# Kernel optimization log

Measured on AMD Instinct MI355X. Metric: run time of the kernel, lower is better.

The kernel has to match this reference:

```python
import jax, jax.numpy as jnp
import numpy as np

N, E = 768, 24576
NODE_DIM, EDGE_DIM, HID = 8, 4, 8
MLP_HID = 4 * HID  # 32


def _mlp(x, params):
    # torch nn.Linear: y = x @ W.T + b; ReLU after every layer except the last
    *hidden, last = params
    for W, b in hidden:
        x = jax.nn.relu(x @ W.T + b)
    W, b = last
    return x @ W.T + b


def _init_mlp(key, dims):
    params = []
    for din, dout in zip(dims[:-1], dims[1:]):
        key, k1, k2 = jax.random.split(key, 3)
        lim = 1.0 / np.sqrt(din)
        W = jax.random.uniform(k1, (dout, din), minval=-lim, maxval=lim, dtype=jnp.float32)
        b = jax.random.uniform(k2, (dout,), minval=-lim, maxval=lim, dtype=jnp.float32)
        params.append((W, b))
    return params


def setup_inputs() -> dict:
    key = jax.random.key(0)
    k_mtr, k_feat, k_ei, k_ea, k_emlp, k_omlp = jax.random.split(key, 6)
    inp = {
        "mtr": jax.random.normal(k_mtr, (N, N, HID), dtype=jnp.float32),
        "feat": jax.random.normal(k_feat, (N, NODE_DIM), dtype=jnp.float32),
        "edge_index": jax.random.randint(k_ei, (2, E), 0, N, dtype=jnp.int64),
        "edge_attr": jax.random.normal(k_ea, (E, EDGE_DIM), dtype=jnp.float32),
    }
    edge_in_dim = EDGE_DIM + 2 * NODE_DIM              # 20
    out_in_dim = 2 * HID + 2 * NODE_DIM + 1            # 33
    eparams = _init_mlp(k_emlp, [edge_in_dim, MLP_HID, MLP_HID, MLP_HID, HID * HID])
    oparams = _init_mlp(k_omlp, [out_in_dim, MLP_HID, MLP_HID, MLP_HID, HID])
    for i, (W, b) in enumerate(eparams):
        inp[f"e_w{i}"], inp[f"e_b{i}"] = W, b
    for i, (W, b) in enumerate(oparams):
        inp[f"o_w{i}"], inp[f"o_b{i}"] = W, b
    return inp


def reference(mtr, feat, edge_index, edge_attr,
              e_w0, e_b0, e_w1, e_b1, e_w2, e_b2, e_w3, e_b3,
              o_w0, o_b0, o_w1, o_b1, o_w2, o_b2, o_w3, o_b3):
    n, h = mtr.shape[0], mtr.shape[2]
    eparams = [(e_w0, e_b0), (e_w1, e_b1), (e_w2, e_b2), (e_w3, e_b3)]
    oparams = [(o_w0, o_b0), (o_w1, o_b1), (o_w2, o_b2), (o_w3, o_b3)]
    src, dst = edge_index[0], edge_index[1]
    # edge MLP on [E, edge_dim + 2*node_dim]
    edge_in = jnp.concatenate([edge_attr, feat[src], feat[dst]], axis=-1)
    evals = _mlp(edge_in, eparams).reshape(-1, h, h)  # [E, h, h]
    # scatter into dense [n, n, h, h] adjacency tensor (zeros for non-edges)
    fmtr = jnp.zeros((n, n, h, h), dtype=mtr.dtype).at[src, dst].set(evals)
    # walk contraction over (j, c)
    mtr1 = jnp.einsum('ijc,jkct->ikt', mtr, fmtr) / h  # [n, n, h]
    eye = jnp.eye(n, dtype=mtr.dtype)[:, :, None]                       # [n, n, 1]
    feat_j = jnp.broadcast_to(feat[None, :, :], (n, n, feat.shape[-1]))  # row-broadcast
    feat_i = jnp.broadcast_to(feat[:, None, :], (n, n, feat.shape[-1]))  # col-broadcast
    cat = jnp.concatenate(
        [mtr1, jnp.transpose(mtr1, (1, 0, 2)), feat_j, feat_i, eye], axis=-1)  # [n, n, 33]
    return mtr + _mlp(cat, oparams)
```

## Files before the change

### kernel.cpp

```cpp
#include <hip/hip_runtime.h>

#define N 768
#define E 24576
#define NPAD_SLOTS (E + 3 * 768)
#define NGROUPS (NPAD_SLOTS / 4)

typedef __attribute__((ext_vector_type(8))) short bf16x8;
typedef __attribute__((ext_vector_type(4))) float f32x4;

__device__ __forceinline__ unsigned pk2(float lo, float hi) {
  unsigned r;
  asm("v_cvt_pk_bf16_f32 %0, %1, %2" : "=v"(r) : "v"(lo), "v"(hi));
  return r;
}

union FragU {
  unsigned u[4];
  bf16x8 s;
};

__device__ __forceinline__ bf16x8 pack_frag(float4 a, float4 b) {
  FragU f;
  f.u[0] = pk2(a.x, a.y);
  f.u[1] = pk2(a.z, a.w);
  f.u[2] = pk2(b.x, b.y);
  f.u[3] = pk2(b.z, b.w);
  return f.s;
}

__device__ __forceinline__ bf16x8 relu_pack(f32x4 d1, f32x4 d2) {
  FragU f;
  f.u[0] = pk2(fmaxf(d1[0], 0.f), fmaxf(d1[1], 0.f));
  f.u[1] = pk2(fmaxf(d1[2], 0.f), fmaxf(d1[3], 0.f));
  f.u[2] = pk2(fmaxf(d2[0], 0.f), fmaxf(d2[1], 0.f));
  f.u[3] = pk2(fmaxf(d2[2], 0.f), fmaxf(d2[3], 0.f));
  return f.s;
}

__device__ __forceinline__ f32x4 ld4(const float* p) {
  float4 v = *(const float4*)p;
  f32x4 r;
  r[0] = v.x; r[1] = v.y; r[2] = v.z; r[3] = v.w;
  return r;
}

__global__ __launch_bounds__(256) void prep0(
    const float* __restrict__ mtr, uint4* __restrict__ mtrT,
    int4* __restrict__ winner4, uint4* __restrict__ Mfrag4,
    int* __restrict__ jlist, int* __restrict__ deg, int* __restrict__ curs,
    int* __restrict__ done_ctr) {
  __shared__ float lds[16][16 * 8 + 4];
  if (blockIdx.x < 2304) {
    const int r = threadIdx.x >> 4;
    const int c = threadIdx.x & 15;
    const size_t j0 = (size_t)(blockIdx.x % 48) * 16;
    const size_t i0 = (size_t)(blockIdx.x / 48) * 16;

    const float4* src = (const float4*)(mtr + ((i0 + r) * N + (j0 + c)) * 8);
    float4 a = src[0], b = src[1];
    *(float4*)&lds[r][c * 8 + 0] = a;
    *(float4*)&lds[r][c * 8 + 4] = b;
    __syncthreads();
    float4 ta = *(float4*)&lds[c][r * 8 + 0];
    float4 tb = *(float4*)&lds[c][r * 8 + 4];
    uint4 o;
    o.x = pk2(ta.x, ta.y); o.y = pk2(ta.z, ta.w);
    o.z = pk2(tb.x, tb.y); o.w = pk2(tb.z, tb.w);
    mtrT[(j0 + r) * N + (i0 + c)] = o;
  } else {
    const int t = (blockIdx.x - 2304) * 256 + threadIdx.x;
    Mfrag4[t] = make_uint4(0, 0, 0, 0);
    if (t < 147456) winner4[t] = make_int4(-1, -1, -1, -1);
    if (t < NPAD_SLOTS) jlist[t] = 0;
    if (t < 1024) { deg[t] = 0; curs[t] = 0; }
    if (t == 0) *done_ctr = 0;
  }
}

__global__ __launch_bounds__(256) void edge_prep_scan(
    const int* __restrict__ ei, int* __restrict__ winner,
    int* __restrict__ deg, int* __restrict__ offs,
    int* __restrict__ done_ctr) {
  const int e = blockIdx.x * 256 + threadIdx.x;
  const int s = ei[e];
  const int d = ei[E + e];
  atomicMax(&winner[(size_t)s * N + d], e);
  atomicAdd(&deg[d], 1);

  __threadfence();
  __syncthreads();
  __shared__ int ticket;
  if (threadIdx.x == 0) ticket = atomicAdd(done_ctr, 1);
  __syncthreads();
  if (ticket == (E / 256) - 1 && threadIdx.x < 64) {
    const int lane = threadIdx.x;
    int v[12];
    int sum = 0;
#pragma unroll
    for (int z = 0; z < 12; ++z) {
      v[z] = (atomicAdd(&deg[lane * 12 + z], 0) + 3) & ~3;
      sum += v[z];
    }
    int inc = sum;
#pragma unroll
    for (int dd = 1; dd < 64; dd <<= 1) {
      int t = __shfl_up(inc, dd, 64);
      if (lane >= dd) inc += t;
    }
    int run = inc - sum;
#pragma unroll
    for (int z = 0; z < 12; ++z) {
      run += v[z];
      offs[lane * 12 + z + 1] = run;
    }
    if (lane == 0) offs[0] = 0;
  }
}

__global__ __launch_bounds__(256) void edge_mlp_mfma(
    const float* __restrict__ feat, const int* __restrict__ ei,
    const float* __restrict__ ea, const int* __restrict__ winner,
    const int* __restrict__ offs, int* __restrict__ curs,
    int* __restrict__ jlist,
    const float* __restrict__ w0, const float* __restrict__ b0,
    const float* __restrict__ w1, const float* __restrict__ b1,
    const float* __restrict__ w2, const float* __restrict__ b2,
    const float* __restrict__ w3, const float* __restrict__ b3,
    short* __restrict__ Mfrag) {
  __shared__ float Ld[4][16 * 65];
  const int wv = threadIdx.x >> 6;
  const int lane = threadIdx.x & 63;
  const int col = lane & 15;
  const int hi = lane >> 4;
  const int e = (blockIdx.x * 4 + wv) * 16 + col;

  const float4 z4 = make_float4(0.f, 0.f, 0.f, 0.f);

  const int s = ei[e];
  const int d = ei[E + e];
  int pos = -1;
  if (hi == 0) {
    if (winner[(size_t)s * N + d] == e) {
      pos = offs[d] + atomicAdd(&curs[d], 1);
      jlist[pos] = s;
    }
  }
  pos = __shfl(pos, col, 64);

  const float* pa = (hi == 0) ? (ea + (size_t)e * 4)
                  : (hi == 1) ? (feat + (size_t)s * 8)
                  : (hi == 2) ? (feat + (size_t)s * 8 + 4)
                              : (feat + (size_t)d * 8);
  float4 va = *(const float4*)pa;
  float4 vb = (hi == 0) ? *(const float4*)(feat + (size_t)d * 8 + 4) : z4;
  bf16x8 bfr = pack_frag(va, vb);

  bf16x8 a0lo, a0hi, a1lo, a1hi, a2lo, a2hi, a3f[4];
  {
    const float* p = w0 + col * 20;
    float4 xa = *(const float4*)(p + hi * 4);
    float4 xb = (hi == 0) ? *(const float4*)(p + 16) : z4;
    a0lo = pack_frag(xa, xb);
    const float* q = w0 + (col + 16) * 20;
    float4 ya = *(const float4*)(q + hi * 4);
    float4 yb = (hi == 0) ? *(const float4*)(q + 16) : z4;
    a0hi = pack_frag(ya, yb);
  }
  a1lo = pack_frag(*(const float4*)(w1 + col * 32 + hi * 4),
                   *(const float4*)(w1 + col * 32 + 16 + hi * 4));
  a1hi = pack_frag(*(const float4*)(w1 + (col + 16) * 32 + hi * 4),
                   *(const float4*)(w1 + (col + 16) * 32 + 16 + hi * 4));
  a2lo = pack_frag(*(const float4*)(w2 + col * 32 + hi * 4),
                   *(const float4*)(w2 + col * 32 + 16 + hi * 4));
  a2hi = pack_frag(*(const float4*)(w2 + (col + 16) * 32 + hi * 4),
                   *(const float4*)(w2 + (col + 16) * 32 + 16 + hi * 4));
#pragma unroll
  for (int q = 0; q < 4; ++q) {
    const float* p = w3 + (size_t)(q * 16 + col) * 32;
    a3f[q] = pack_frag(*(const float4*)(p + hi * 4),
                       *(const float4*)(p + 16 + hi * 4));
  }

  f32x4 d1 = ld4(b0 + hi * 4), d2 = ld4(b0 + 16 + hi * 4);
  d1 = __builtin_amdgcn_mfma_f32_16x16x32_bf16(a0lo, bfr, d1, 0, 0, 0);
  d2 = __builtin_amdgcn_mfma_f32_16x16x32_bf16(a0hi, bfr, d2, 0, 0, 0);
  bfr = relu_pack(d1, d2);

  d1 = ld4(b1 + hi * 4); d2 = ld4(b1 + 16 + hi * 4);
  d1 = __builtin_amdgcn_mfma_f32_16x16x32_bf16(a1lo, bfr, d1, 0, 0, 0);
  d2 = __builtin_amdgcn_mfma_f32_16x16x32_bf16(a1hi, bfr, d2, 0, 0, 0);
  bfr = relu_pack(d1, d2);

  d1 = ld4(b2 + hi * 4); d2 = ld4(b2 + 16 + hi * 4);
  d1 = __builtin_amdgcn_mfma_f32_16x16x32_bf16(a2lo, bfr, d1, 0, 0, 0);
  d2 = __builtin_amdgcn_mfma_f32_16x16x32_bf16(a2hi, bfr, d2, 0, 0, 0);
  bfr = relu_pack(d1, d2);

#pragma unroll
  for (int q = 0; q < 4; ++q) {
    f32x4 d3 = ld4(b3 + q * 16 + hi * 4);
    d3 = __builtin_amdgcn_mfma_f32_16x16x32_bf16(a3f[q], bfr, d3, 0, 0, 0);
#pragma unroll
    for (int r = 0; r < 4; ++r)
      Ld[wv][col * 65 + q * 16 + hi * 4 + r] = d3[r];
  }
  __syncthreads();

  if (pos >= 0) {
    const int gid = pos >> 2;
    const int sg = pos & 3;
    short* base = Mfrag + (size_t)gid * 512 + (sg & 1) * 256 + (sg >> 1) * 4;
    const int hl = hi >> 1;
    const int t0 = (hi & 1) * 4;
    const float* m = &Ld[wv][col * 65];
#pragma unroll
    for (int cc = 0; cc < 4; ++cc) {
      const int t = t0 + cc;
      unsigned u0 = pk2(m[(hl * 4 + 0) * 8 + t], m[(hl * 4 + 1) * 8 + t]);
      unsigned u1 = pk2(m[(hl * 4 + 2) * 8 + t], m[(hl * 4 + 3) * 8 + t]);
      *(uint2*)(base + hl * 128 + t * 8) = make_uint2(u0, u1);
    }
  }
}

__global__ __launch_bounds__(256) void contract7(
    const short* __restrict__ mtrT, const short* __restrict__ Mfrag,
    const int* __restrict__ jlist, const int* __restrict__ offs,
    const int* __restrict__ wcnt, short* __restrict__ WTb) {
  __shared__ float sD[4][4][16][9];

  const int bid = blockIdx.x;
  const int g = (bid & 7) * 288 + (bid >> 3);
  const int ig = g / 768;
  const int k = g % 768;
  const int w = threadIdx.x >> 6;
  const int lane = threadIdx.x & 63;
  const int col = lane & 15;
  const int hi = lane >> 4;
  const int ibase = ig * 256 + w * 64;

  const int base = offs[k];
  const int cnt = wcnt[k];
  const int ngr = (cnt + 3) >> 2;

  f32x4 acc0 = {0.f, 0.f, 0.f, 0.f}, acc1 = {0.f, 0.f, 0.f, 0.f};
  f32x4 acc2 = {0.f, 0.f, 0.f, 0.f}, acc3 = {0.f, 0.f, 0.f, 0.f};

  const size_t lane_off = ((size_t)(ibase + col)) * 8 + (hi & 1) * 4;

#pragma unroll 1
  for (int gg = 0; gg < ngr; ++gg) {
    const int4 js = *(const int4*)(jlist + base + gg * 4);
    const int ja = (hi & 2) ? js.y : js.x;
    const int jb = (hi & 2) ? js.w : js.z;

    bf16x8 bfr = *(const bf16x8*)(
        Mfrag + ((size_t)(base >> 2) + gg) * 512 + lane * 8);

    const short* pa = mtrT + (size_t)ja * (N * 8) + lane_off;
    const short* pb = mtrT + (size_t)jb * (N * 8) + lane_off;

#define TILE(ACC, T)                                                     \
  do {                                                                   \
    uint2 ua = *(const uint2*)(pa + (T) * (16 * 8));                     \
    uint2 ub = *(const uint2*)(pb + (T) * (16 * 8));                     \
    FragU af;                                                            \
    af.u[0] = ua.x; af.u[1] = ua.y; af.u[2] = ub.x; af.u[3] = ub.y;      \
    ACC = __builtin_amdgcn_mfma_f32_16x16x32_bf16(af.s, bfr, ACC, 0, 0, 0); \
  } while (0)

    TILE(acc0, 0);
    TILE(acc1, 1);
    TILE(acc2, 2);
    TILE(acc3, 3);
#undef TILE
  }

  if (col < 8) {
#pragma unroll
    for (int r = 0; r < 4; ++r) {
      sD[w][0][hi * 4 + r][col] = acc0[r] * 0.125f;
      sD[w][1][hi * 4 + r][col] = acc1[r] * 0.125f;
      sD[w][2][hi * 4 + r][col] = acc2[r] * 0.125f;
      sD[w][3][hi * 4 + r][col] = acc3[r] * 0.125f;
    }
  }
  __syncthreads();
  if (lane < 16) {
#pragma unroll
    for (int t = 0; t < 4; ++t) {
      const float* row = &sD[w][t][lane][0];
      uint4 o;
      o.x = pk2(row[0], row[1]); o.y = pk2(row[2], row[3]);
      o.z = pk2(row[4], row[5]); o.w = pk2(row[6], row[7]);
      *(uint4*)(WTb + ((size_t)k * N + ibase + t * 16 + lane) * 8) = o;
    }
  }
}

__global__ __launch_bounds__(256, 2) void out_mlp_mfma(
    const float* __restrict__ mtr, const short* __restrict__ WTb,
    const float* __restrict__ feat,
    const float* __restrict__ w0, const float* __restrict__ b0,
    const float* __restrict__ w1, const float* __restrict__ b1,
    const float* __restrict__ w2, const float* __restrict__ b2,
    const float* __restrict__ w3, const float* __restrict__ b3,
    float* __restrict__ out) {
  const int i = blockIdx.x;
  const int w = threadIdx.x >> 6;
  const int col = threadIdx.x & 15;
  const int hi = (threadIdx.x >> 4) & 3;

  bf16x8 a0lo, a0hi, a1lo, a1hi, a2lo, a2hi, a3;
  {
    const float* p = w0 + col * 33;
    float4 xa = make_float4(p[hi * 4], p[hi * 4 + 1], p[hi * 4 + 2], p[hi * 4 + 3]);
    float4 xb = make_float4(p[16 + hi * 4], p[16 + hi * 4 + 1],
                            p[16 + hi * 4 + 2], p[16 + hi * 4 + 3]);
    a0lo = pack_frag(xa, xb);
    const float* q = w0 + (col + 16) * 33;
    float4 ya = make_float4(q[hi * 4], q[hi * 4 + 1], q[hi * 4 + 2], q[hi * 4 + 3]);
    float4 yb = make_float4(q[16 + hi * 4], q[16 + hi * 4 + 1],
                            q[16 + hi * 4 + 2], q[16 + hi * 4 + 3]);
    a0hi = pack_frag(ya, yb);
  }
  a1lo = pack_frag(*(const float4*)(w1 + col * 32 + hi * 4),
                   *(const float4*)(w1 + col * 32 + 16 + hi * 4));
  a1hi = pack_frag(*(const float4*)(w1 + (col + 16) * 32 + hi * 4),
                   *(const float4*)(w1 + (col + 16) * 32 + 16 + hi * 4));
  a2lo = pack_frag(*(const float4*)(w2 + col * 32 + hi * 4),
                   *(const float4*)(w2 + col * 32 + 16 + hi * 4));
  a2hi = pack_frag(*(const float4*)(w2 + (col + 16) * 32 + hi * 4),
                   *(const float4*)(w2 + (col + 16) * 32 + 16 + hi * 4));
  if (col < 8) {
    a3 = pack_frag(*(const float4*)(w3 + col * 32 + hi * 4),
                   *(const float4*)(w3 + col * 32 + 16 + hi * 4));
  } else {
    FragU z; z.u[0] = z.u[1] = z.u[2] = z.u[3] = 0; a3 = z.s;
  }

  const f32x4 c1a = ld4(b0 + hi * 4), c1b = ld4(b0 + 16 + hi * 4);
  const f32x4 c2a = ld4(b1 + hi * 4), c2b = ld4(b1 + 16 + hi * 4);
  const f32x4 c3a = ld4(b2 + hi * 4), c3b = ld4(b2 + 16 + hi * 4);
  f32x4 c4;
  if (hi < 2) c4 = ld4(b3 + hi * 4);
  else { c4[0] = c4[1] = c4[2] = c4[3] = 0.f; }

  float dg1[4], dg2[4];
#pragma unroll
  for (int r = 0; r < 4; ++r) {
    dg1[r] = w0[(hi * 4 + r) * 33 + 32];
    dg2[r] = w0[(16 + hi * 4 + r) * 33 + 32];
  }

#pragma unroll 1
  for (int g = 0; g < 12; ++g) {
    const int krow = w * 192 + g * 16 + col;

    FragU bf;
    const short* pW = (hi < 2)
        ? (WTb + ((size_t)krow * N + i) * 8 + (hi & 1) * 4)
        : (WTb + ((size_t)i * N + krow) * 8 + (hi & 1) * 4);
    uint2 wv2 = *(const uint2*)pW;
    const float* pF = (hi < 2) ? (feat + (size_t)krow * 8 + (hi & 1) * 4)
                               : (feat + (size_t)i * 8 + (hi & 1) * 4);
    float4 fv = *(const float4*)pF;
    bf.u[0] = wv2.x; bf.u[1] = wv2.y;
    bf.u[2] = pk2(fv.x, fv.y); bf.u[3] = pk2(fv.z, fv.w);
    bf16x8 bfr = bf.s;

    f32x4 d1 = c1a, d2 = c1b;
    d1 = __builtin_amdgcn_mfma_f32_16x16x32_bf16(a0lo, bfr, d1, 0, 0, 0);
    d2 = __builtin_amdgcn_mfma_f32_16x16x32_bf16(a0hi, bfr, d2, 0, 0, 0);
    const float eye = (krow == i) ? 1.f : 0.f;
#pragma unroll
    for (int r = 0; r < 4; ++r) {
      d1[r] = fmaf(eye, dg1[r], d1[r]);
      d2[r] = fmaf(eye, dg2[r], d2[r]);
    }
    bfr = relu_pack(d1, d2);

    d1 = c2a; d2 = c2b;
    d1 = __builtin_amdgcn_mfma_f32_16x16x32_bf16(a1lo, bfr, d1, 0, 0, 0);
    d2 = __builtin_amdgcn_mfma_f32_16x16x32_bf16(a1hi, bfr, d2, 0, 0, 0);
    bfr = relu_pack(d1, d2);

    d1 = c3a; d2 = c3b;
    d1 = __builtin_amdgcn_mfma_f32_16x16x32_bf16(a2lo, bfr, d1, 0, 0, 0);
    d2 = __builtin_amdgcn_mfma_f32_16x16x32_bf16(a2hi, bfr, d2, 0, 0, 0);
    bfr = relu_pack(d1, d2);

    f32x4 d3 = c4;
    d3 = __builtin_amdgcn_mfma_f32_16x16x32_bf16(a3, bfr, d3, 0, 0, 0);

    if (hi < 2) {
      const size_t idx = ((size_t)i * N + krow) * 8 + hi * 4;
      float4 m = *(const float4*)(mtr + idx);
      *(float4*)(out + idx) =
          make_float4(m.x + d3[0], m.y + d3[1], m.z + d3[2], m.w + d3[3]);
    }
  }
}

extern "C" void kernel_launch(void* const* d_in, const int* in_sizes, int n_in,
                              void* d_out, int out_size, void* d_ws,
                              size_t ws_size, hipStream_t stream) {
  const float* mtr  = (const float*)d_in[0];
  const float* feat = (const float*)d_in[1];
  const int*   ei   = (const int*)d_in[2];
  const float* ea   = (const float*)d_in[3];
  const float* ew0 = (const float*)d_in[4];
  const float* eb0 = (const float*)d_in[5];
  const float* ew1 = (const float*)d_in[6];
  const float* eb1 = (const float*)d_in[7];
  const float* ew2 = (const float*)d_in[8];
  const float* eb2 = (const float*)d_in[9];
  const float* ew3 = (const float*)d_in[10];
  const float* eb3 = (const float*)d_in[11];
  const float* ow0 = (const float*)d_in[12];
  const float* ob0 = (const float*)d_in[13];
  const float* ow1 = (const float*)d_in[14];
  const float* ob1 = (const float*)d_in[15];
  const float* ow2 = (const float*)d_in[16];
  const float* ob2 = (const float*)d_in[17];
  const float* ow3 = (const float*)d_in[18];
  const float* ob3 = (const float*)d_in[19];
  float* out = (float*)d_out;

  char* ws = (char*)d_ws;
  short* Mfrag = (short*)ws; ws += (size_t)NGROUPS * 512 * 2;
  short* mtrT  = (short*)ws; ws += (size_t)N * N * 8 * 2;
  short* WTb   = (short*)ws; ws += (size_t)N * N * 8 * 2;
  int* winner  = (int*)ws;   ws += (size_t)N * N * 4;
  int* deg     = (int*)ws;   ws += 1024 * 4;
  int* offs    = (int*)ws;   ws += 1024 * 4;
  int* curs    = (int*)ws;   ws += 1024 * 4;
  int* done_ctr = (int*)ws;  ws += 256 * 4;
  int* jlist   = (int*)ws;   ws += (size_t)NPAD_SLOTS * 4;

  prep0<<<2304 + 1680, 256, 0, stream>>>(mtr, (uint4*)mtrT, (int4*)winner,
                                         (uint4*)Mfrag, jlist, deg, curs,
                                         done_ctr);
  edge_prep_scan<<<E / 256, 256, 0, stream>>>(ei, winner, deg, offs, done_ctr);
  edge_mlp_mfma<<<E / 64, 256, 0, stream>>>(feat, ei, ea, winner, offs, curs,
                                            jlist, ew0, eb0, ew1, eb1, ew2,
                                            eb2, ew3, eb3, Mfrag);
  contract7<<<2304, 256, 0, stream>>>(mtrT, Mfrag, jlist, offs, curs, WTb);
  out_mlp_mfma<<<N, 256, 0, stream>>>(mtr, WTb, feat, ow0, ob0, ow1, ob1, ow2,
                                      ob2, ow3, ob3, out);
}
```

Measured before the change: 91.08 us.

## Fuse contraction and output MLP into persistent kernel with grid barrier and prefetch

Merges the contract and out_mlp kernels into one persistent kernel of 768 blocks. Each block does three contraction work items, then waits at a software grid barrier built from atomics before running the output MLP. The contraction loop now software-pipelines its gathers of the j-list, mtrT and Mfrag one group ahead. The MLP loop prefetches the WTb, feat and residual mtr values for the next row group. This removes one launch and hides load latency, but the spin barrier assumes all 768 blocks are resident at once (launch bounds of 3 per CU), and a larger register footprint may reduce occupancy.

```diff
diff --git a/kernel.cpp b/kernel.cpp
--- a/kernel.cpp
+++ b/kernel.cpp
@@ -4,6 +4,7 @@
 #define E 24576
 #define NPAD_SLOTS (E + 3 * 768)
 #define NGROUPS (NPAD_SLOTS / 4)
+#define TAIL_NB 768
 
 typedef __attribute__((ext_vector_type(8))) short bf16x8;
 typedef __attribute__((ext_vector_type(4))) float f32x4;
@@ -44,11 +45,25 @@
   return r;
 }
 
+__device__ __forceinline__ void grid_barrier(int* cnt, int* flag) {
+  __syncthreads();
+  __threadfence();
+  if (threadIdx.x == 0) {
+    if (atomicAdd(cnt, 1) == TAIL_NB - 1) {
+      atomicExch(flag, 1);
+    } else {
+      while (atomicAdd(flag, 0) == 0) __builtin_amdgcn_s_sleep(16);
+    }
+  }
+  __syncthreads();
+  __threadfence();
+}
+
 __global__ __launch_bounds__(256) void prep0(
     const float* __restrict__ mtr, uint4* __restrict__ mtrT,
     int4* __restrict__ winner4, uint4* __restrict__ Mfrag4,
     int* __restrict__ jlist, int* __restrict__ deg, int* __restrict__ curs,
-    int* __restrict__ done_ctr) {
+    int* __restrict__ ctrs) {
   __shared__ float lds[16][16 * 8 + 4];
   if (blockIdx.x < 2304) {
     const int r = threadIdx.x >> 4;
@@ -73,7 +88,7 @@
     if (t < 147456) winner4[t] = make_int4(-1, -1, -1, -1);
     if (t < NPAD_SLOTS) jlist[t] = 0;
     if (t < 1024) { deg[t] = 0; curs[t] = 0; }
-    if (t == 0) *done_ctr = 0;
+    if (t < 8) ctrs[t] = 0;
   }
 }
 
@@ -223,93 +238,120 @@
   }
 }
 
-__global__ __launch_bounds__(256) void contract7(
+__global__ __launch_bounds__(256, 3) void tail_fused(
     const short* __restrict__ mtrT, const short* __restrict__ Mfrag,
     const int* __restrict__ jlist, const int* __restrict__ offs,
-    const int* __restrict__ wcnt, short* __restrict__ WTb) {
+    const int* __restrict__ wcnt, short* __restrict__ WTb,
+    const float* __restrict__ mtr, const float* __restrict__ feat,
+    const float* __restrict__ w0, const float* __restrict__ b0,
+    const float* __restrict__ w1, const float* __restrict__ b1,
+    const float* __restrict__ w2, const float* __restrict__ b2,
+    const float* __restrict__ w3, const float* __restrict__ b3,
+    float* __restrict__ out, int* __restrict__ bar_cnt,
+    int* __restrict__ bar_flag) {
   __shared__ float sD[4][4][16][9];
 
-  const int bid = blockIdx.x;
-  const int g = (bid & 7) * 288 + (bid >> 3);
-  const int ig = g / 768;
-  const int k = g % 768;
   const int w = threadIdx.x >> 6;
   const int lane = threadIdx.x & 63;
   const int col = lane & 15;
   const int hi = lane >> 4;
-  const int ibase = ig * 256 + w * 64;
-
-  const int base = offs[k];
-  const int cnt = wcnt[k];
-  const int ngr = (cnt + 3) >> 2;
-
-  f32x4 acc0 = {0.f, 0.f, 0.f, 0.f}, acc1 = {0.f, 0.f, 0.f, 0.f};
-  f32x4 acc2 = {0.f, 0.f, 0.f, 0.f}, acc3 = {0.f, 0.f, 0.f, 0.f};
-
-  const size_t lane_off = ((size_t)(ibase + col)) * 8 + (hi & 1) * 4;
 
 #pragma unroll 1
-  for (int gg = 0; gg < ngr; ++gg) {
-    const int4 js = *(const int4*)(jlist + base + gg * 4);
-    const int ja = (hi & 2) ? js.y : js.x;
-    const int jb = (hi & 2) ? js.w : js.z;
-
-    bf16x8 bfr = *(const bf16x8*)(
-        Mfrag + ((size_t)(base >> 2) + gg) * 512 + lane * 8);
-
-    const short* pa = mtrT + (size_t)ja * (N * 8) + lane_off;
-    const short* pb = mtrT + (size_t)jb * (N * 8) + lane_off;
-
-#define TILE(ACC, T)                                                     \
-  do {                                                                   \
-    uint2 ua = *(const uint2*)(pa + (T) * (16 * 8));                     \
-    uint2 ub = *(const uint2*)(pb + (T) * (16 * 8));                     \
-    FragU af;                                                            \
-    af.u[0] = ua.x; af.u[1] = ua.y; af.u[2] = ub.x; af.u[3] = ub.y;      \
-    ACC = __builtin_amdgcn_mfma_f32_16x16x32_bf16(af.s, bfr, ACC, 0, 0, 0); \
+  for (int it = 0; it < 3; ++it) {
+    const int vb = blockIdx.x + it * TAIL_NB;
+    const int g = (vb & 7) * 288 + (vb >> 3);
+    const int ig = g / 768;
+    const int k = g % 768;
+    const int ibase = ig * 256 + w * 64;
+
+    const int base = offs[k];
+    const int cnt = wcnt[k];
+    const int ngr = (cnt + 3) >> 2;
+
+    f32x4 acc0 = {0.f, 0.f, 0.f, 0.f}, acc1 = {0.f, 0.f, 0.f, 0.f};
+    f32x4 acc2 = {0.f, 0.f, 0.f, 0.f}, acc3 = {0.f, 0.f, 0.f, 0.f};
+
+    const size_t lane_off = ((size_t)(ibase + col)) * 8 + (hi & 1) * 4;
+    const short* Mf = Mfrag + (size_t)(base >> 2) * 512 + lane * 8;
+
+#define LOADA(JS, AA, AB)                                               \
+  do {                                                                  \
+    const int _ja = (hi & 2) ? (JS).y : (JS).x;                         \
+    const int _jb = (hi & 2) ? (JS).w : (JS).z;                         \
+    const short* _pa = mtrT + (size_t)_ja * (N * 8) + lane_off;         \
+    const short* _pb = mtrT + (size_t)_jb * (N * 8) + lane_off;         \
+    _Pragma("unroll") for (int t = 0; t < 4; ++t) {                     \
+      AA[t] = *(const uint2*)(_pa + t * 128);                           \
+      AB[t] = *(const uint2*)(_pb + t * 128);                           \
+    }                                                                   \
   } while (0)
 
-    TILE(acc0, 0);
-    TILE(acc1, 1);
-    TILE(acc2, 2);
-    TILE(acc3, 3);
+    uint2 Aa0[4], Ab0[4], Aa1[4], Ab1[4];
+    bf16x8 mb0, mb1;
+    int4 js1 = make_int4(0, 0, 0, 0);
+
+    {
+      int4 js0 = *(const int4*)(jlist + base);
+      if (ngr > 1) js1 = *(const int4*)(jlist + base + 4);
+      LOADA(js0, Aa0, Ab0);
+      mb0 = *(const bf16x8*)(Mf);
+    }
+
+#pragma unroll 1
+    for (int gg = 0; gg < ngr; ++gg) {
+      int4 js2 = js1;
+      if (gg + 2 < ngr) js2 = *(const int4*)(jlist + base + (gg + 2) * 4);
+      if (gg + 1 < ngr) {
+        LOADA(js1, Aa1, Ab1);
+        mb1 = *(const bf16x8*)(Mf + (size_t)(gg + 1) * 512);
+      }
+
+#define TILE(ACC, T)                                                       \
+  do {                                                                    \
+    FragU af;                                                             \
+    af.u[0] = Aa0[T].x; af.u[1] = Aa0[T].y;                               \
+    af.u[2] = Ab0[T].x; af.u[3] = Ab0[T].y;                               \
+    ACC = __builtin_amdgcn_mfma_f32_16x16x32_bf16(af.s, mb0, ACC, 0, 0, 0); \
+  } while (0)
+      TILE(acc0, 0);
+      TILE(acc1, 1);
+      TILE(acc2, 2);
+      TILE(acc3, 3);
 #undef TILE
-  }
-
-  if (col < 8) {
-#pragma unroll
-    for (int r = 0; r < 4; ++r) {
-      sD[w][0][hi * 4 + r][col] = acc0[r] * 0.125f;
-      sD[w][1][hi * 4 + r][col] = acc1[r] * 0.125f;
-      sD[w][2][hi * 4 + r][col] = acc2[r] * 0.125f;
-      sD[w][3][hi * 4 + r][col] = acc3[r] * 0.125f;
-    }
-  }
-  __syncthreads();
-  if (lane < 16) {
-#pragma unroll
-    for (int t = 0; t < 4; ++t) {
-      const float* row = &sD[w][t][lane][0];
-      uint4 o;
-      o.x = pk2(row[0], row[1]); o.y = pk2(row[2], row[3]);
-      o.z = pk2(row[4], row[5]); o.w = pk2(row[6], row[7]);
-      *(uint4*)(WTb + ((size_t)k * N + ibase + t * 16 + lane) * 8) = o;
-    }
-  }
-}
-
-__global__ __launch_bounds__(256, 2) void out_mlp_mfma(
-    const float* __restrict__ mtr, const short* __restrict__ WTb,
-    const float* __restrict__ feat,
-    const float* __restrict__ w0, const float* __restrict__ b0,
-    const float* __restrict__ w1, const float* __restrict__ b1,
-    const float* __restrict__ w2, const float* __restrict__ b2,
-    const float* __restrict__ w3, const float* __restrict__ b3,
-    float* __restrict__ out) {
+
+      js1 = js2;
+#pragma unroll
+      for (int t = 0; t < 4; ++t) { Aa0[t] = Aa1[t]; Ab0[t] = Ab1[t]; }
+      mb0 = mb1;
+    }
+#undef LOADA
+
+    if (col < 8) {
+#pragma unroll
+      for (int r = 0; r < 4; ++r) {
+        sD[w][0][hi * 4 + r][col] = acc0[r] * 0.125f;
+        sD[w][1][hi * 4 + r][col] = acc1[r] * 0.125f;
+        sD[w][2][hi * 4 + r][col] = acc2[r] * 0.125f;
+        sD[w][3][hi * 4 + r][col] = acc3[r] * 0.125f;
+      }
+    }
+    __syncthreads();
+    if (lane < 16) {
+#pragma unroll
+      for (int t = 0; t < 4; ++t) {
+        const float* row = &sD[w][t][lane][0];
+        uint4 o;
+        o.x = pk2(row[0], row[1]); o.y = pk2(row[2], row[3]);
+        o.z = pk2(row[4], row[5]); o.w = pk2(row[6], row[7]);
+        *(uint4*)(WTb + ((size_t)k * N + ibase + t * 16 + lane) * 8) = o;
+      }
+    }
+    __syncthreads();
+  }
+
+  grid_barrier(bar_cnt, bar_flag);
+
   const int i = blockIdx.x;
-  const int w = threadIdx.x >> 6;
-  const int col = threadIdx.x & 15;
-  const int hi = (threadIdx.x >> 4) & 3;
 
   bf16x8 a0lo, a0hi, a1lo, a1hi, a2lo, a2hi, a3;
   {
@@ -353,18 +395,36 @@
     dg2[r] = w0[(16 + hi * 4 + r) * 33 + 32];
   }
 
+#define PW(G) ((hi < 2) ? (WTb + ((size_t)(w * 192 + (G) * 16 + col) * N + i) * 8 + (hi & 1) * 4) \
+                        : (WTb + ((size_t)i * N + (w * 192 + (G) * 16 + col)) * 8 + (hi & 1) * 4))
+#define PF(G) ((hi < 2) ? (feat + (size_t)(w * 192 + (G) * 16 + col) * 8 + (hi & 1) * 4) \
+                        : (feat + (size_t)i * 8 + (hi & 1) * 4))
+
+  uint2 wv2 = *(const uint2*)PW(0);
+  float4 fv = *(const float4*)PF(0);
+  float4 mres;
+  if (hi < 2) {
+    const size_t idx0 = ((size_t)i * N + (w * 192 + col)) * 8 + hi * 4;
+    mres = *(const float4*)(mtr + idx0);
+  }
+
 #pragma unroll 1
   for (int g = 0; g < 12; ++g) {
     const int krow = w * 192 + g * 16 + col;
 
+    uint2 wv2n = wv2;
+    float4 fvn = fv;
+    float4 mresn = mres;
+    if (g + 1 < 12) {
+      wv2n = *(const uint2*)PW(g + 1);
+      fvn = *(const float4*)PF(g + 1);
+      if (hi < 2) {
+        const size_t idxn = ((size_t)i * N + (krow + 16)) * 8 + hi * 4;
+        mresn = *(const float4*)(mtr + idxn);
+      }
+    }
+
     FragU bf;
-    const short* pW = (hi < 2)
-        ? (WTb + ((size_t)krow * N + i) * 8 + (hi & 1) * 4)
-        : (WTb + ((size_t)i * N + krow) * 8 + (hi & 1) * 4);
-    uint2 wv2 = *(const uint2*)pW;
-    const float* pF = (hi < 2) ? (feat + (size_t)krow * 8 + (hi & 1) * 4)
-                               : (feat + (size_t)i * 8 + (hi & 1) * 4);
-    float4 fv = *(const float4*)pF;
     bf.u[0] = wv2.x; bf.u[1] = wv2.y;
     bf.u[2] = pk2(fv.x, fv.y); bf.u[3] = pk2(fv.z, fv.w);
     bf16x8 bfr = bf.s;
@@ -395,11 +455,16 @@
 
     if (hi < 2) {
       const size_t idx = ((size_t)i * N + krow) * 8 + hi * 4;
-      float4 m = *(const float4*)(mtr + idx);
-      *(float4*)(out + idx) =
-          make_float4(m.x + d3[0], m.y + d3[1], m.z + d3[2], m.w + d3[3]);
-    }
-  }
+      *(float4*)(out + idx) = make_float4(mres.x + d3[0], mres.y + d3[1],
+                                          mres.z + d3[2], mres.w + d3[3]);
+    }
+
+    wv2 = wv2n;
+    fv = fvn;
+    mres = mresn;
+  }
+#undef PW
+#undef PF
 }
 
 extern "C" void kernel_launch(void* const* d_in, const int* in_sizes, int n_in,
@@ -435,17 +500,18 @@
   int* deg     = (int*)ws;   ws += 1024 * 4;
   int* offs    = (int*)ws;   ws += 1024 * 4;
   int* curs    = (int*)ws;   ws += 1024 * 4;
-  int* done_ctr = (int*)ws;  ws += 256 * 4;
+  int* ctrs    = (int*)ws;   ws += 256 * 4;
   int* jlist   = (int*)ws;   ws += (size_t)NPAD_SLOTS * 4;
 
   prep0<<<2304 + 1680, 256, 0, stream>>>(mtr, (uint4*)mtrT, (int4*)winner,
                                          (uint4*)Mfrag, jlist, deg, curs,
-                                         done_ctr);
-  edge_prep_scan<<<E / 256, 256, 0, stream>>>(ei, winner, deg, offs, done_ctr);
+                                         ctrs);
+  edge_prep_scan<<<E / 256, 256, 0, stream>>>(ei, winner, deg, offs, &ctrs[0]);
   edge_mlp_mfma<<<E / 64, 256, 0, stream>>>(feat, ei, ea, winner, offs, curs,
                                             jlist, ew0, eb0, ew1, eb1, ew2,
                                             eb2, ew3, eb3, Mfrag);
-  contract7<<<2304, 256, 0, stream>>>(mtrT, Mfrag, jlist, offs, curs, WTb);
-  out_mlp_mfma<<<N, 256, 0, stream>>>(mtr, WTb, feat, ow0, ob0, ow1, ob1, ow2,
-                                      ob2, ow3, ob3, out);
-}
+  tail_fused<<<TAIL_NB, 256, 0, stream>>>(mtrT, Mfrag, jlist, offs, curs, WTb,
+                                          mtr, feat, ow0, ob0, ow1, ob1, ow2,
+                                          ob2, ow3, ob3, out, &ctrs[1],
+                                          &ctrs[2]);
+}
```

After: 259.0 us. 184% more time.
